# Kernel tuning notes

Measured on AMD Instinct MI355X. Metric: run time of the kernel, lower is better.

## Reference

```python
import jax, jax.numpy as jnp
import numpy as np

_MIN_BLOCK_KV = 32


def setup_inputs() -> dict:
    key = jax.random.key(0)
    k0, k1, k2, k3 = jax.random.split(key, 4)
    B, H, HKV, D, T, S = 32, 32, 8, 128, 2048, 8
    pool = B * T
    q = jax.random.normal(k0, (B, H, D), dtype=jnp.float32)
    k_buffer = jax.random.normal(k1, (pool, HKV, D), dtype=jnp.float32)
    v_buffer = jax.random.normal(k2, (pool, HKV, D), dtype=jnp.float32)
    # uniform contexts: request b owns tokens [b*T, (b+1)*T) of the pool, in permuted (paged) order
    kv_indptr = (jnp.arange(B + 1, dtype=jnp.int32) * T)
    kv_indices = jax.random.permutation(k3, pool).astype(jnp.int32)
    num_kv_splits = jnp.full((B,), S, dtype=jnp.int32)
    return {"q": q, "k_buffer": k_buffer, "v_buffer": v_buffer,
            "kv_indptr": kv_indptr, "kv_indices": kv_indices,
            "num_kv_splits": num_kv_splits}


def reference(q, k_buffer, v_buffer, kv_indptr, kv_indices, num_kv_splits):
    # Paged KV-cache decode attention, stage 1 (split-KV partial softmax).
    B, H, D = q.shape
    HKV = k_buffer.shape[1]
    Lv = v_buffer.shape[-1]
    G = H // HKV                       # GQA group size
    sm_scale = 1.0 / (D ** 0.5)        # Model default (sm_scale=None)
    logit_cap = 0.0                    # Model default -> capping disabled

    seq_lens = kv_indptr[1:] - kv_indptr[:-1]          # [B]
    T = kv_indices.shape[0] // B                       # max context len (uniform setup)
    S = int(jnp.max(num_kv_splits))                    # max_kv_splits (eager, as in torch code)

    pos = jnp.arange(T, dtype=jnp.int32)               # [T]
    valid = pos[None, :] < seq_lens[:, None]           # [B,T]
    # gather KV pool locations per (batch, position); clamp OOB positions
    gidx = kv_indptr[:-1, None] + jnp.minimum(pos[None, :], seq_lens[:, None] - 1)
    kv_loc = kv_indices[gidx]                          # [B,T]
    k_g = k_buffer[kv_loc]                             # [B,T,HKV,D]
    v_g = v_buffer[kv_loc]                             # [B,T,HKV,Lv]

    qr = q.reshape(B, HKV, G, D)
    qk = jnp.einsum('bkgd,btkd->bkgt', qr, k_g) * sm_scale   # [B,HKV,G,T]
    if logit_cap > 0:
        qk = logit_cap * jnp.tanh(qk / logit_cap)

    # split assignment: kv_len_per_split = cdiv(cdiv(seq_len, splits), MIN) * MIN
    cdiv = lambda a, b: (a + b - 1) // b
    kv_len_per_split = cdiv(cdiv(seq_lens, num_kv_splits), _MIN_BLOCK_KV) * _MIN_BLOCK_KV  # [B]
    split_id = pos[None, :] // kv_len_per_split[:, None]      # [B,T]
    split_mask = (split_id[:, None, :] == jnp.arange(S, dtype=jnp.int32)[None, :, None]) \
                 & valid[:, None, :]                          # [B,S,T]

    neg_inf = jnp.float32(-jnp.inf)
    masked = jnp.where(split_mask[:, None, None, :, :], qk[:, :, :, None, :], neg_inf)  # [B,HKV,G,S,T]
    m = jnp.max(masked, axis=-1)                               # [B,HKV,G,S]
    m_safe = jnp.where(jnp.isfinite(m), m, 0.0)                # guard empty splits
    p = jnp.exp(masked - m_safe[..., None])                    # [B,HKV,G,S,T]
    p = jnp.where(split_mask[:, None, None, :, :], p, 0.0)
    e_sum = jnp.sum(p, axis=-1)                                # [B,HKV,G,S]
    acc = jnp.einsum('bkgst,btkv->bkgsv', p, v_g)              # [B,HKV,G,S,Lv]

    att_out = (acc / e_sum[..., None]).reshape(B, H, S, Lv)
    att_lse = (m + jnp.log(e_sum)).reshape(B, H, S)
    return att_out, att_lse
```

## Files before the change

### kernel.cpp

```cpp
#include <hip/hip_runtime.h>
#include <math.h>


namespace {
constexpr int kB = 32;
constexpr int kH = 32;
constexpr int kHKV = 8;
constexpr int kD = 128;
constexpr int kG = kH / kHKV;
constexpr int kS = 8;
constexpr int kMinBlockKV = 32;
}

__global__ __launch_bounds__(256, 2) void decode_split_kernel(
    const float* __restrict__ q,
    const float* __restrict__ k_buffer,
    const float* __restrict__ v_buffer,
    const int* __restrict__ kv_indptr,
    const int* __restrict__ kv_indices,
    const int* __restrict__ num_kv_splits,
    float* __restrict__ att_out,
    float* __restrict__ att_lse)
{
    const int bid = blockIdx.x;
    const int s  = bid % kS;
    const int kh = (bid / kS) % kHKV;
    const int b  = bid / (kS * kHKV);

    const int tid  = threadIdx.x;
    const int wave = tid >> 6;
    const int lane = tid & 63;
    const int tg   = lane >> 4;
    const int li   = lane & 15;

    const int ptr0    = kv_indptr[b];
    const int seq_len = kv_indptr[b + 1] - ptr0;
    const int splits  = num_kv_splits[b];
    const int per     = (seq_len + splits - 1) / splits;
    const int lps     = ((per + kMinBlockKV - 1) / kMinBlockKV) * kMinBlockKV;
    const int t0 = s * lps;
    const int t1 = min(t0 + lps, seq_len);

    const float sm_scale = 0.08838834764831845f;

    float4 q0[kG], q1[kG];
    const float* qb = q + ((size_t)b * kH + (size_t)kh * kG) * kD;
    #pragma unroll
    for (int g = 0; g < kG; ++g) {
        float4 a = *(const float4*)(qb + (size_t)g * kD + li * 4);
        float4 c = *(const float4*)(qb + (size_t)g * kD + 64 + li * 4);
        q0[g] = make_float4(a.x * sm_scale, a.y * sm_scale, a.z * sm_scale, a.w * sm_scale);
        q1[g] = make_float4(c.x * sm_scale, c.y * sm_scale, c.z * sm_scale, c.w * sm_scale);
    }

    float  l[kG] = {0.f, 0.f, 0.f, 0.f};
    float4 a0[kG], a1[kG];
    #pragma unroll
    for (int g = 0; g < kG; ++g) {
        a0[g] = make_float4(0.f, 0.f, 0.f, 0.f);
        a1[g] = make_float4(0.f, 0.f, 0.f, 0.f);
    }

    for (int base = t0 + wave * 64; base < t1; base += 256) {
        const int nt = min(64, t1 - base);
        int my_loc = 0;
        if (lane < nt) my_loc = kv_indices[ptr0 + base + lane];
        const int ng = (nt + 3) >> 2;

        float4 k0a, k1a, v0a, v1a;
        float4 k0b, k1b, v0b, v1b;
        float4 k0c, k1c, v0c, v1c;
        float4 k0d, k1d, v0d, v1d;

#define LOADG(PIG, K0, K1, V0, V1)                                          \
        {                                                                   \
            const int _loc = __shfl(my_loc, min((PIG) * 4 + tg, nt - 1));   \
            const float* _kb = k_buffer + ((size_t)_loc * kHKV + kh) * kD;  \
            const float* _vb = v_buffer + ((size_t)_loc * kHKV + kh) * kD;  \
            K0 = *(const float4*)(_kb + li * 4);                            \
            K1 = *(const float4*)(_kb + 64 + li * 4);                       \
            V0 = *(const float4*)(_vb + li * 4);                            \
            V1 = *(const float4*)(_vb + 64 + li * 4);                       \
        }

#define COMPUTE(CIG, K0, K1, V0, V1)                                        \
        {                                                                   \
            float dot[kG];                                                  \
            _Pragma("unroll")                                               \
            for (int g = 0; g < kG; ++g) {                                  \
                float d = q0[g].x * K0.x;                                   \
                d = fmaf(q0[g].y, K0.y, d);                                 \
                d = fmaf(q0[g].z, K0.z, d);                                 \
                d = fmaf(q0[g].w, K0.w, d);                                 \
                d = fmaf(q1[g].x, K1.x, d);                                 \
                d = fmaf(q1[g].y, K1.y, d);                                 \
                d = fmaf(q1[g].z, K1.z, d);                                 \
                d = fmaf(q1[g].w, K1.w, d);                                 \
                dot[g] = d;                                                 \
            }                                                               \
            _Pragma("unroll")                                               \
            for (int m = 1; m <= 8; m <<= 1) {                              \
                _Pragma("unroll")                                           \
                for (int g = 0; g < kG; ++g)                                \
                    dot[g] += __shfl_xor(dot[g], m);                        \
            }                                                               \
            const bool valid = ((CIG) * 4 + tg) < nt;                       \
            _Pragma("unroll")                                               \
            for (int g = 0; g < kG; ++g) {                                  \
                const float p = valid ? __expf(dot[g]) : 0.f;               \
                l[g] += p;                                                  \
                a0[g].x = fmaf(p, V0.x, a0[g].x);                           \
                a0[g].y = fmaf(p, V0.y, a0[g].y);                           \
                a0[g].z = fmaf(p, V0.z, a0[g].z);                           \
                a0[g].w = fmaf(p, V0.w, a0[g].w);                           \
                a1[g].x = fmaf(p, V1.x, a1[g].x);                           \
                a1[g].y = fmaf(p, V1.y, a1[g].y);                           \
                a1[g].z = fmaf(p, V1.z, a1[g].z);                           \
                a1[g].w = fmaf(p, V1.w, a1[g].w);                           \
            }                                                               \
        }

        LOADG(0, k0a, k1a, v0a, v1a)
        LOADG(1, k0b, k1b, v0b, v1b)
        LOADG(2, k0c, k1c, v0c, v1c)

        for (int ig = 0; ig < ng; ig += 4) {
            LOADG(ig + 3, k0d, k1d, v0d, v1d)
            COMPUTE(ig,     k0a, k1a, v0a, v1a)
            LOADG(ig + 4, k0a, k1a, v0a, v1a)
            COMPUTE(ig + 1, k0b, k1b, v0b, v1b)
            LOADG(ig + 5, k0b, k1b, v0b, v1b)
            COMPUTE(ig + 2, k0c, k1c, v0c, v1c)
            LOADG(ig + 6, k0c, k1c, v0c, v1c)
            COMPUTE(ig + 3, k0d, k1d, v0d, v1d)
        }
#undef LOADG
#undef COMPUTE
    }

    #pragma unroll
    for (int m = 16; m <= 32; m <<= 1) {
        #pragma unroll
        for (int g = 0; g < kG; ++g) {
            a0[g].x += __shfl_xor(a0[g].x, m);
            a0[g].y += __shfl_xor(a0[g].y, m);
            a0[g].z += __shfl_xor(a0[g].z, m);
            a0[g].w += __shfl_xor(a0[g].w, m);
            a1[g].x += __shfl_xor(a1[g].x, m);
            a1[g].y += __shfl_xor(a1[g].y, m);
            a1[g].z += __shfl_xor(a1[g].z, m);
            a1[g].w += __shfl_xor(a1[g].w, m);
            l[g] += __shfl_xor(l[g], m);
        }
    }

    __shared__ float s_acc[4][kG][kD];
    __shared__ float s_l[4][kG];
    if (tg == 0) {
        #pragma unroll
        for (int g = 0; g < kG; ++g) {
            *(float4*)&s_acc[wave][g][li * 4]      = a0[g];
            *(float4*)&s_acc[wave][g][64 + li * 4] = a1[g];
        }
        if (li == 0) {
            #pragma unroll
            for (int g = 0; g < kG; ++g) s_l[wave][g] = l[g];
        }
    }
    __syncthreads();

    const int g = tid >> 6;
    const int d = (tid & 63) * 2;
    float o0 = 0.f, o1 = 0.f, ls = 0.f;
    #pragma unroll
    for (int w = 0; w < 4; ++w) {
        o0 += s_acc[w][g][d];
        o1 += s_acc[w][g][d + 1];
        ls += s_l[w][g];
    }
    const float inv = 1.0f / ls;
    const size_t hidx = (size_t)b * kH + (size_t)kh * kG + g;
    float* outp = att_out + (hidx * kS + s) * kD + d;
    outp[0] = o0 * inv;
    outp[1] = o1 * inv;
    if ((tid & 63) == 0)
        att_lse[hidx * kS + s] = logf(ls);
}

extern "C" void kernel_launch(void* const* d_in, const int* in_sizes, int n_in,
                              void* d_out, int out_size, void* d_ws, size_t ws_size,
                              hipStream_t stream) {
    const float* q             = (const float*)d_in[0];
    const float* k_buffer      = (const float*)d_in[1];
    const float* v_buffer      = (const float*)d_in[2];
    const int*   kv_indptr     = (const int*)d_in[3];
    const int*   kv_indices    = (const int*)d_in[4];
    const int*   num_kv_splits = (const int*)d_in[5];

    float* att_out = (float*)d_out;
    float* att_lse = att_out + (size_t)kB * kH * kS * kD;

    dim3 grid(kB * kHKV * kS);
    decode_split_kernel<<<grid, 256, 0, stream>>>(
        q, k_buffer, v_buffer, kv_indptr, kv_indices, num_kv_splits,
        att_out, att_lse);
}
```

Before: 531.7 us.

## Stage K/V tiles through LDS with async global_load_lds triple buffering

Replaces the register-based four-deep software prefetch with direct global-to-LDS asynchronous loads (global_load_lds, 16 bytes per lane) into a per-wave three-slot ring buffer. Explicit vmcnt and lgkmcnt waits plus sched barriers control the pipeline, and the reduction scratch is aliased onto the staging buffer. The aim is to cut the VGPR pressure of holding prefetched K/V in registers while keeping enough loads in flight to hide gather latency. In exchange it adds an LDS round trip for every K/V element and uses fewer in-flight groups than before, and the hand-written waitcnt counts must stay correct.

Result: no change. 533.3 us (+0.3%).

```diff
diff --git a/kernel.cpp b/kernel.cpp
--- a/kernel.cpp
+++ b/kernel.cpp
@@ -10,6 +10,14 @@
 constexpr int kG = kH / kHKV;
 constexpr int kS = 8;
 constexpr int kMinBlockKV = 32;
+constexpr int kDepth = 3;
+}
+
+__device__ __forceinline__ void gload16(const float* g, float* l) {
+    __builtin_amdgcn_global_load_lds(
+        (const __attribute__((address_space(1))) void*)g,
+        (__attribute__((address_space(3))) void*)l,
+        16, 0, 0);
 }
 
 __global__ __launch_bounds__(256, 2) void decode_split_kernel(
@@ -43,6 +51,8 @@
 
     const float sm_scale = 0.08838834764831845f;
 
+    __shared__ float stage[4][kDepth][2][512];
+
     float4 q0[kG], q1[kG];
     const float* qb = q + ((size_t)b * kH + (size_t)kh * kG) * kD;
     #pragma unroll
@@ -67,75 +77,84 @@
         if (lane < nt) my_loc = kv_indices[ptr0 + base + lane];
         const int ng = (nt + 3) >> 2;
 
-        float4 k0a, k1a, v0a, v1a;
-        float4 k0b, k1b, v0b, v1b;
-        float4 k0c, k1c, v0c, v1c;
-        float4 k0d, k1d, v0d, v1d;
-
-#define LOADG(PIG, K0, K1, V0, V1)                                          \
-        {                                                                   \
-            const int _loc = __shfl(my_loc, min((PIG) * 4 + tg, nt - 1));   \
-            const float* _kb = k_buffer + ((size_t)_loc * kHKV + kh) * kD;  \
-            const float* _vb = v_buffer + ((size_t)_loc * kHKV + kh) * kD;  \
-            K0 = *(const float4*)(_kb + li * 4);                            \
-            K1 = *(const float4*)(_kb + 64 + li * 4);                       \
-            V0 = *(const float4*)(_vb + li * 4);                            \
-            V1 = *(const float4*)(_vb + 64 + li * 4);                       \
-        }
-
-#define COMPUTE(CIG, K0, K1, V0, V1)                                        \
-        {                                                                   \
-            float dot[kG];                                                  \
-            _Pragma("unroll")                                               \
-            for (int g = 0; g < kG; ++g) {                                  \
-                float d = q0[g].x * K0.x;                                   \
-                d = fmaf(q0[g].y, K0.y, d);                                 \
-                d = fmaf(q0[g].z, K0.z, d);                                 \
-                d = fmaf(q0[g].w, K0.w, d);                                 \
-                d = fmaf(q1[g].x, K1.x, d);                                 \
-                d = fmaf(q1[g].y, K1.y, d);                                 \
-                d = fmaf(q1[g].z, K1.z, d);                                 \
-                d = fmaf(q1[g].w, K1.w, d);                                 \
-                dot[g] = d;                                                 \
-            }                                                               \
-            _Pragma("unroll")                                               \
-            for (int m = 1; m <= 8; m <<= 1) {                              \
-                _Pragma("unroll")                                           \
-                for (int g = 0; g < kG; ++g)                                \
-                    dot[g] += __shfl_xor(dot[g], m);                        \
-            }                                                               \
-            const bool valid = ((CIG) * 4 + tg) < nt;                       \
-            _Pragma("unroll")                                               \
-            for (int g = 0; g < kG; ++g) {                                  \
-                const float p = valid ? __expf(dot[g]) : 0.f;               \
-                l[g] += p;                                                  \
-                a0[g].x = fmaf(p, V0.x, a0[g].x);                           \
-                a0[g].y = fmaf(p, V0.y, a0[g].y);                           \
-                a0[g].z = fmaf(p, V0.z, a0[g].z);                           \
-                a0[g].w = fmaf(p, V0.w, a0[g].w);                           \
-                a1[g].x = fmaf(p, V1.x, a1[g].x);                           \
-                a1[g].y = fmaf(p, V1.y, a1[g].y);                           \
-                a1[g].z = fmaf(p, V1.z, a1[g].z);                           \
-                a1[g].w = fmaf(p, V1.w, a1[g].w);                           \
-            }                                                               \
-        }
-
-        LOADG(0, k0a, k1a, v0a, v1a)
-        LOADG(1, k0b, k1b, v0b, v1b)
-        LOADG(2, k0c, k1c, v0c, v1c)
-
-        for (int ig = 0; ig < ng; ig += 4) {
-            LOADG(ig + 3, k0d, k1d, v0d, v1d)
-            COMPUTE(ig,     k0a, k1a, v0a, v1a)
-            LOADG(ig + 4, k0a, k1a, v0a, v1a)
-            COMPUTE(ig + 1, k0b, k1b, v0b, v1b)
-            LOADG(ig + 5, k0b, k1b, v0b, v1b)
-            COMPUTE(ig + 2, k0c, k1c, v0c, v1c)
-            LOADG(ig + 6, k0c, k1c, v0c, v1c)
-            COMPUTE(ig + 3, k0d, k1d, v0d, v1d)
-        }
-#undef LOADG
-#undef COMPUTE
+#define ISSUE(IG)                                                            \
+        {                                                                    \
+            const int _ig   = (IG);                                          \
+            const int _slot = _ig % kDepth;                                  \
+            const int _pair = lane >> 5;                                     \
+            const int _o32  = (lane & 31) * 4;                               \
+            const int _iA = min(_ig * 4 + _pair,     nt - 1);                \
+            const int _iB = min(_ig * 4 + 2 + _pair, nt - 1);                \
+            const int _lA = __shfl(my_loc, _iA);                             \
+            const int _lB = __shfl(my_loc, _iB);                             \
+            const size_t _rA = ((size_t)_lA * kHKV + kh) * kD;               \
+            const size_t _rB = ((size_t)_lB * kHKV + kh) * kD;               \
+            gload16(k_buffer + _rA + _o32, &stage[wave][_slot][0][0]);       \
+            gload16(k_buffer + _rB + _o32, &stage[wave][_slot][0][256]);     \
+            gload16(v_buffer + _rA + _o32, &stage[wave][_slot][1][0]);       \
+            gload16(v_buffer + _rB + _o32, &stage[wave][_slot][1][256]);     \
+        }
+
+        if (ng > 0) ISSUE(0)
+        if (ng > 1) ISSUE(1)
+        if (ng > 2) ISSUE(2)
+
+        for (int ig = 0; ig < ng; ++ig) {
+            const int slot = ig % kDepth;
+            const int rem  = ng - 1 - ig;
+            if (rem >= 2)      asm volatile("s_waitcnt vmcnt(8)" ::: "memory");
+            else if (rem == 1) asm volatile("s_waitcnt vmcnt(4)" ::: "memory");
+            else               asm volatile("s_waitcnt vmcnt(0)" ::: "memory");
+            __builtin_amdgcn_sched_barrier(0);
+
+            const float* kp = &stage[wave][slot][0][tg * 128];
+            const float* vp = &stage[wave][slot][1][tg * 128];
+            float4 ck0 = *(const float4*)(kp + li * 4);
+            float4 ck1 = *(const float4*)(kp + 64 + li * 4);
+            float4 cv0 = *(const float4*)(vp + li * 4);
+            float4 cv1 = *(const float4*)(vp + 64 + li * 4);
+
+            asm volatile("s_waitcnt lgkmcnt(0)" ::: "memory");
+            __builtin_amdgcn_sched_barrier(0);
+
+            if (ig + kDepth < ng) ISSUE(ig + kDepth)
+
+            float dot[kG];
+            #pragma unroll
+            for (int g = 0; g < kG; ++g) {
+                float d = q0[g].x * ck0.x;
+                d = fmaf(q0[g].y, ck0.y, d);
+                d = fmaf(q0[g].z, ck0.z, d);
+                d = fmaf(q0[g].w, ck0.w, d);
+                d = fmaf(q1[g].x, ck1.x, d);
+                d = fmaf(q1[g].y, ck1.y, d);
+                d = fmaf(q1[g].z, ck1.z, d);
+                d = fmaf(q1[g].w, ck1.w, d);
+                dot[g] = d;
+            }
+            #pragma unroll
+            for (int m = 1; m <= 8; m <<= 1) {
+                #pragma unroll
+                for (int g = 0; g < kG; ++g)
+                    dot[g] += __shfl_xor(dot[g], m);
+            }
+
+            const bool valid = (ig * 4 + tg) < nt;
+            #pragma unroll
+            for (int g = 0; g < kG; ++g) {
+                const float p = valid ? __expf(dot[g]) : 0.f;
+                l[g] += p;
+                a0[g].x = fmaf(p, cv0.x, a0[g].x);
+                a0[g].y = fmaf(p, cv0.y, a0[g].y);
+                a0[g].z = fmaf(p, cv0.z, a0[g].z);
+                a0[g].w = fmaf(p, cv0.w, a0[g].w);
+                a1[g].x = fmaf(p, cv1.x, a1[g].x);
+                a1[g].y = fmaf(p, cv1.y, a1[g].y);
+                a1[g].z = fmaf(p, cv1.z, a1[g].z);
+                a1[g].w = fmaf(p, cv1.w, a1[g].w);
+            }
+        }
+#undef ISSUE
     }
 
     #pragma unroll
@@ -154,17 +173,18 @@
         }
     }
 
-    __shared__ float s_acc[4][kG][kD];
-    __shared__ float s_l[4][kG];
+    __syncthreads();
+    float* s_acc = &stage[0][0][0][0];
+    float* s_l   = s_acc + 4 * kG * kD;
     if (tg == 0) {
         #pragma unroll
         for (int g = 0; g < kG; ++g) {
-            *(float4*)&s_acc[wave][g][li * 4]      = a0[g];
-            *(float4*)&s_acc[wave][g][64 + li * 4] = a1[g];
+            *(float4*)&s_acc[(wave * kG + g) * kD + li * 4]      = a0[g];
+            *(float4*)&s_acc[(wave * kG + g) * kD + 64 + li * 4] = a1[g];
         }
         if (li == 0) {
             #pragma unroll
-            for (int g = 0; g < kG; ++g) s_l[wave][g] = l[g];
+            for (int g = 0; g < kG; ++g) s_l[wave * kG + g] = l[g];
         }
     }
     __syncthreads();
@@ -174,9 +194,9 @@
     float o0 = 0.f, o1 = 0.f, ls = 0.f;
     #pragma unroll
     for (int w = 0; w < 4; ++w) {
-        o0 += s_acc[w][g][d];
-        o1 += s_acc[w][g][d + 1];
-        ls += s_l[w][g];
+        o0 += s_acc[(w * kG + g) * kD + d];
+        o1 += s_acc[(w * kG + g) * kD + d + 1];
+        ls += s_l[w * kG + g];
     }
     const float inv = 1.0f / ls;
     const size_t hidx = (size_t)b * kH + (size_t)kh * kG + g;
```
